# Kernel optimization log

Hardware: AMD Instinct MI355X
Metric: run time of the kernel (lower is better)

Reference implementation:

```python
import jax, jax.numpy as jnp
import numpy as np

B, N, D, H = 2, 2048, 1024, 16
HD = D // H  # 64
EPS = 1e-6


def setup_inputs() -> dict:
    key = jax.random.key(0)
    ks = jax.random.split(key, 16)
    rnd = lambda k, shp: jax.random.normal(k, shp, dtype=jnp.float32)
    w = lambda k, i, o: rnd(k, (i, o)) * 0.02  # stored as (in, out); y = x @ W
    return {
        "x": rnd(ks[0], (B, N, D)),
        "emb_B_D": rnd(ks[1], (B, D)),
        "gate": rnd(ks[2], (B, D)),
        "crossattn_emb": rnd(ks[3], (B, 128, D)),
        "rope_emb_L_1_1_D": rnd(ks[4], (N, HD)),
        "Wq1": w(ks[5], D, D), "Wq2": w(ks[6], D, D),
        "Wk1": w(ks[7], D, D), "Wk2": w(ks[8], D, D),
        "Wv": w(ks[9], D, D),
        "Wo": w(ks[10], D, D),
        "Wada1": w(ks[11], D, D),
        "Wada2": w(ks[12], D, 2 * D),
        "bada2": jnp.zeros((2 * D,), dtype=jnp.float32),
    }


def rotate_half(t):
    t1, t2 = jnp.split(t, 2, axis=-1)
    return jnp.concatenate([-t2, t1], axis=-1)


def reference(x, emb_B_D, gate, crossattn_emb, rope_emb_L_1_1_D,
              Wq1, Wq2, Wk1, Wk2, Wv, Wo, Wada1, Wada2, bada2):
    # adaLN modulation: SiLU -> Linear(no bias) -> Linear(bias)
    ada = jax.nn.silu(emb_B_D) @ Wada1 @ Wada2 + bada2          # [B, 2D]
    shift, scale = jnp.split(ada, 2, axis=1)                    # [B, D] each

    # LayerNorm (no affine) + scale/shift
    mu = jnp.mean(x, axis=-1, keepdims=True)
    var = jnp.var(x, axis=-1, keepdims=True)
    xn = (x - mu) * jax.lax.rsqrt(var + EPS)
    xn = xn * (1.0 + scale[:, None, :]) + shift[:, None, :]     # [B, N, D]

    # QKV projections (each to_q/to_k is two stacked linears, to_v one)
    q = xn @ Wq1 @ Wq2
    k = xn @ Wk1 @ Wk2
    v = xn @ Wv
    split_heads = lambda t: t.reshape(B, N, H, HD).transpose(0, 2, 1, 3)  # b h n d
    q, k, v = split_heads(q), split_heads(k), split_heads(v)

    # RoPE
    cos = jnp.cos(rope_emb_L_1_1_D)[None, None]                 # [1,1,N,HD]
    sin = jnp.sin(rope_emb_L_1_1_D)[None, None]
    q = q * cos + rotate_half(q) * sin
    k = k * cos + rotate_half(k) * sin

    # Attention
    sim = jnp.einsum("bhid,bhjd->bhij", q, k) * (HD ** -0.5)
    attn = jax.nn.softmax(sim, axis=-1)
    out = jnp.einsum("bhij,bhjd->bhid", attn, v)
    out = out.transpose(0, 2, 1, 3).reshape(B, N, D) @ Wo

    # Gated residual
    return x + gate[:, None, :] * out
```

## Files before the change

### kernel.cpp

```cpp
#include <hip/hip_runtime.h>
#include <stdint.h>
#include <math.h>

typedef unsigned short u16;
typedef __attribute__((ext_vector_type(8))) short short8;
typedef __attribute__((ext_vector_type(4))) float f32x4;
typedef __attribute__((ext_vector_type(4))) unsigned short u16x4;
typedef __attribute__((ext_vector_type(2))) unsigned int uint2v;

#define DEV static __device__ __forceinline__

DEV u16 f2bf(float f) {
    unsigned u = __builtin_bit_cast(unsigned, f);
    u = u + 0x7fffu + ((u >> 16) & 1u);
    return (u16)(u >> 16);
}
DEV float bf2f(u16 s) { return __builtin_bit_cast(float, ((unsigned)s) << 16); }
DEV unsigned pk2(float a, float b) {
    unsigned ua = __builtin_bit_cast(unsigned, a) + 0x8000u;
    unsigned ub = __builtin_bit_cast(unsigned, b) + 0x8000u;
    return (ua >> 16) | (ub & 0xffff0000u);
}
DEV float fexp2(float x) {
#if __has_builtin(__builtin_amdgcn_exp2f)
    return __builtin_amdgcn_exp2f(x);
#else
    return __expf(x * 0.69314718056f);
#endif
}

DEV void gl_lds16(const u16* g, u16* l) {
#if __has_builtin(__builtin_amdgcn_global_load_lds)
    __builtin_amdgcn_global_load_lds((const __attribute__((address_space(1))) unsigned int*)g,
                                     (__attribute__((address_space(3))) unsigned int*)l, 16, 0, 0);
#else
    *(short8*)l = *(const short8*)g;
#endif
}


__global__ __launch_bounds__(256) void k_ada1(const float* __restrict__ emb, const float* __restrict__ W,
                                              float* __restrict__ out) {
    int col = blockIdx.x * 64 + (threadIdx.x & 63);
    int b = blockIdx.y;
    int kbase = blockIdx.z * 128 + (threadIdx.x >> 6) * 32;
    float acc = 0.f;
    for (int k = kbase; k < kbase + 32; k++) {
        float e = emb[b * 1024 + k];
        float se = e / (1.f + __expf(-e));
        acc += se * W[(size_t)k * 1024 + col];
    }
    __shared__ float red[4][64];
    red[threadIdx.x >> 6][threadIdx.x & 63] = acc;
    __syncthreads();
    if (threadIdx.x < 64)
        atomicAdd(out + b * 1024 + blockIdx.x * 64 + threadIdx.x,
                  red[0][threadIdx.x] + red[1][threadIdx.x] + red[2][threadIdx.x] + red[3][threadIdx.x]);
}

__global__ __launch_bounds__(256) void k_prep(const float* s0, u16* d0, const float* s1, u16* d1,
                                              const float* s2, u16* d2, const float* s3, u16* d3,
                                              const float* s4, u16* d4, const float* s5, u16* d5,
                                              const float* __restrict__ t_ada, const float* __restrict__ Wada2,
                                              float* __restrict__ ada, const float* __restrict__ rope,
                                              float* __restrict__ cst, float* __restrict__ snt) {
    __shared__ u16 tile[64][65];
    __shared__ float red[4][64];
    if (blockIdx.z == 6) {
        int flat = blockIdx.y * 16 + blockIdx.x;
        int kq = flat >> 6;
        int rest = flat & 63;
        int b = rest >> 5, xb = rest & 31;
        int col = xb * 64 + (threadIdx.x & 63);
        int kbase = kq * 256 + (threadIdx.x >> 6) * 64;
        float acc = 0.f;
        for (int k = kbase; k < kbase + 64; k++)
            acc += t_ada[b * 1024 + k] * Wada2[(size_t)k * 2048 + col];
        red[threadIdx.x >> 6][threadIdx.x & 63] = acc;
        __syncthreads();
        if (threadIdx.x < 64)
            atomicAdd(ada + b * 2048 + xb * 64 + threadIdx.x,
                      red[0][threadIdx.x] + red[1][threadIdx.x] + red[2][threadIdx.x] + red[3][threadIdx.x]);
        return;
    }
    if (blockIdx.z == 7) {
        int flat = blockIdx.y * 16 + blockIdx.x;
        if (flat < 128) {
            int idx = flat * 1024 + threadIdx.x * 4;
            float4 rv = *(const float4*)(rope + idx);
            float4 cv, sv;
            __sincosf(rv.x, &sv.x, &cv.x);
            __sincosf(rv.y, &sv.y, &cv.y);
            __sincosf(rv.z, &sv.z, &cv.z);
            __sincosf(rv.w, &sv.w, &cv.w);
            *(float4*)(cst + idx) = cv;
            *(float4*)(snt + idx) = sv;
        }
        return;
    }
    const float* s; u16* d;
    switch (blockIdx.z) {
        case 0: s = s0; d = d0; break;
        case 1: s = s1; d = d1; break;
        case 2: s = s2; d = d2; break;
        case 3: s = s3; d = d3; break;
        case 4: s = s4; d = d4; break;
        default: s = s5; d = d5; break;
    }
    int k0 = blockIdx.x * 64, n0 = blockIdx.y * 64;
    int tx = threadIdx.x & 63, ty = threadIdx.x >> 6;
    if (blockIdx.z >= 4) {
        #pragma unroll
        for (int i = 0; i < 16; i++) {
            int kk = ty + 4 * i;
            d[(size_t)(k0 + kk) * 1024 + n0 + tx] = f2bf(s[(size_t)(k0 + kk) * 1024 + n0 + tx]);
        }
        return;
    }
    #pragma unroll
    for (int i = 0; i < 16; i++) {
        int kk = ty + 4 * i;
        tile[kk][tx] = f2bf(s[(size_t)(k0 + kk) * 1024 + n0 + tx]);
    }
    __syncthreads();
    #pragma unroll
    for (int i = 0; i < 16; i++) {
        int nn = ty + 4 * i;
        d[(size_t)(n0 + nn) * 1024 + k0 + tx] = tile[tx][nn];
    }
}

__global__ __launch_bounds__(256) void k_ln(const float* __restrict__ x, const float* __restrict__ ada,
                                            const float* __restrict__ bada2, u16* __restrict__ xn) {
    int row = blockIdx.x;
    int b = row >> 11;
    float4 v = ((const float4*)(x + (size_t)row * 1024))[threadIdx.x];
    float s = v.x + v.y + v.z + v.w;
    float ss = v.x * v.x + v.y * v.y + v.z * v.z + v.w * v.w;
    #pragma unroll
    for (int m = 1; m < 64; m <<= 1) { s += __shfl_xor(s, m, 64); ss += __shfl_xor(ss, m, 64); }
    __shared__ float red[2][4];
    int wave = threadIdx.x >> 6, lane = threadIdx.x & 63;
    if (lane == 0) { red[0][wave] = s; red[1][wave] = ss; }
    __syncthreads();
    s = red[0][0] + red[0][1] + red[0][2] + red[0][3];
    ss = red[1][0] + red[1][1] + red[1][2] + red[1][3];
    float mu = s * (1.f / 1024.f);
    float var = ss * (1.f / 1024.f) - mu * mu;
    float rs = rsqrtf(var + 1e-6f);
    int c = threadIdx.x * 4;
    const float* sh = ada + b * 2048;
    const float* sc = ada + b * 2048 + 1024;
    u16x4 r;
    r.x = f2bf((v.x - mu) * rs * (1.f + sc[c + 0] + bada2[1024 + c + 0]) + sh[c + 0] + bada2[c + 0]);
    r.y = f2bf((v.y - mu) * rs * (1.f + sc[c + 1] + bada2[1024 + c + 1]) + sh[c + 1] + bada2[c + 1]);
    r.z = f2bf((v.z - mu) * rs * (1.f + sc[c + 2] + bada2[1024 + c + 2]) + sh[c + 2] + bada2[c + 2]);
    r.w = f2bf((v.w - mu) * rs * (1.f + sc[c + 3] + bada2[1024 + c + 3]) + sh[c + 3] + bada2[c + 3]);
    *(u16x4*)(xn + (size_t)row * 1024 + c) = r;
}

template <int BM, int BN, int MODE>
DEV void gemm_core(const u16* __restrict__ A, const u16* __restrict__ Bt,
                   u16* __restrict__ Cb, float* __restrict__ Cf, u16* __restrict__ Vt,
                   const float* __restrict__ Xres, const float* __restrict__ gate,
                   const float* __restrict__ cst, const float* __restrict__ snt,
                   float scale, int Nn, int K, int m0, int n0) {
    constexpr int MI = BM / 32, NJ = BN / 32;
    constexpr int PA = BM / 64, PB = BN / 64;
    constexpr int LA = BM * 40, LB = BN * 40;
    __shared__ u16 smem[2 * (LA + LB)];
    int tid = threadIdx.x;
    int lane = tid & 63, wave = tid >> 6;
    int wm = (wave & 1) * (BM / 2), wn = (wave >> 1) * (BN / 2);
    int lr = lane & 15, quad = lane >> 4;
    f32x4 acc[MI][NJ];
    #pragma unroll
    for (int i = 0; i < MI; i++)
        #pragma unroll
        for (int j = 0; j < NJ; j++) acc[i][j] = f32x4{0.f, 0.f, 0.f, 0.f};

    int arow = tid >> 2;
    int achunk = (tid & 3) * 8;
    const u16* ap = A + (size_t)(m0 + arow) * K + achunk;
    const u16* bp = Bt + (size_t)(n0 + arow) * K + achunk;
    u16* AsL[2] = { smem, smem + LA };
    u16* BsL[2] = { smem + 2 * LA, smem + 2 * LA + LB };

    short8 ra[2][PA], rb[2][PB];
    #pragma unroll
    for (int p = 0; p < PA; p++) ra[0][p] = *(const short8*)(ap + (size_t)(64 * p) * K);
    #pragma unroll
    for (int p = 0; p < PB; p++) rb[0][p] = *(const short8*)(bp + (size_t)(64 * p) * K);
    #pragma unroll
    for (int p = 0; p < PA; p++) *(short8*)(&AsL[0][(arow + 64 * p) * 40 + achunk]) = ra[0][p];
    #pragma unroll
    for (int p = 0; p < PB; p++) *(short8*)(&BsL[0][(arow + 64 * p) * 40 + achunk]) = rb[0][p];
    #pragma unroll
    for (int p = 0; p < PA; p++) ra[1][p] = *(const short8*)(ap + 32 + (size_t)(64 * p) * K);
    #pragma unroll
    for (int p = 0; p < PB; p++) rb[1][p] = *(const short8*)(bp + 32 + (size_t)(64 * p) * K);
    __syncthreads();

    auto body = [&](int it, int cur) {
        if (it + 2 < 32) {
            int koff = (it + 2) * 32;
            #pragma unroll
            for (int p = 0; p < PA; p++) ra[cur][p] = *(const short8*)(ap + koff + (size_t)(64 * p) * K);
            #pragma unroll
            for (int p = 0; p < PB; p++) rb[cur][p] = *(const short8*)(bp + koff + (size_t)(64 * p) * K);
        }
        short8 af[MI], bfr[NJ];
        #pragma unroll
        for (int i = 0; i < MI; i++) af[i] = *(const short8*)(&AsL[cur][(wm + i * 16 + lr) * 40 + quad * 8]);
        #pragma unroll
        for (int j = 0; j < NJ; j++) bfr[j] = *(const short8*)(&BsL[cur][(wn + j * 16 + lr) * 40 + quad * 8]);
        #pragma unroll
        for (int i = 0; i < MI; i++)
            #pragma unroll
            for (int j = 0; j < NJ; j++)
                acc[i][j] = __builtin_amdgcn_mfma_f32_16x16x32_bf16(af[i], bfr[j], acc[i][j], 0, 0, 0);
        if (it + 1 < 32) {
            int nxt = cur ^ 1;
            #pragma unroll
            for (int p = 0; p < PA; p++) *(short8*)(&AsL[nxt][(arow + 64 * p) * 40 + achunk]) = ra[nxt][p];
            #pragma unroll
            for (int p = 0; p < PB; p++) *(short8*)(&BsL[nxt][(arow + 64 * p) * 40 + achunk]) = rb[nxt][p];
        }
        __syncthreads();
    };
    #pragma unroll 1
    for (int it2 = 0; it2 < 16; ++it2) {
        body(2 * it2, 0);
        body(2 * it2 + 1, 1);
    }

    if (MODE == 2) {
        if ((n0 + wn) < 2048) {
            #pragma unroll
            for (int i = 0; i < MI; i++)
                #pragma unroll
                for (int jp = 0; jp < 2; jp++)
                    #pragma unroll
                    for (int r = 0; r < 4; r++) {
                        int row = m0 + wm + i * 16 + quad * 4 + r;
                        int n = row & 2047;
                        int d1 = jp * 16 + lr;
                        float c1 = cst[n * 64 + d1],      s1 = snt[n * 64 + d1];
                        float c2 = cst[n * 64 + d1 + 32], s2 = snt[n * 64 + d1 + 32];
                        float x1 = acc[i][jp][r], x2 = acc[i][jp + 2][r];
                        Cb[(size_t)row * Nn + n0 + wn + d1]      = f2bf(x1 * c1 - x2 * s1);
                        Cb[(size_t)row * Nn + n0 + wn + d1 + 32] = f2bf(x2 * c2 + x1 * s2);
                    }
        } else {
            #pragma unroll
            for (int i = 0; i < MI; i++)
                #pragma unroll
                for (int j = 0; j < NJ; j++) {
                    u16x4 w;
                    w.x = f2bf(acc[i][j][0]); w.y = f2bf(acc[i][j][1]);
                    w.z = f2bf(acc[i][j][2]); w.w = f2bf(acc[i][j][3]);
                    *(u16x4*)(&smem[(wn + j * 16 + lr) * 132 + wm + i * 16 + quad * 4]) = w;
                }
            __syncthreads();
            int d = tid >> 1, half = tid & 1;
            int gcol = n0 - 2048 + d;
            int hv = gcol >> 6, dl = gcol & 63;
            int bb = m0 >> 11;
            int nloc = (m0 & 2047) + half * 64;
            u16* dst = Vt + ((size_t)((bb * 16 + hv) * 64 + dl)) * 2048 + nloc;
            #pragma unroll
            for (int c = 0; c < 8; c++)
                *(short8*)(dst + c * 8) = *(const short8*)(&smem[d * 132 + half * 64 + c * 8]);
        }
        return;
    }
    #pragma unroll
    for (int i = 0; i < MI; i++)
        #pragma unroll
        for (int j = 0; j < NJ; j++)
            #pragma unroll
            for (int r = 0; r < 4; r++) {
                int row = m0 + wm + i * 16 + quad * 4 + r;
                int col = n0 + wn + j * 16 + lr;
                float v = acc[i][j][r];
                if (MODE == 1) {
                    int b = row >> 11;
                    Cf[(size_t)row * Nn + col] = Xres[(size_t)row * Nn + col] + gate[b * 1024 + col] * v;
                } else {
                    Cb[(size_t)row * Nn + col] = f2bf(v * scale);
                }
            }
}

template <int BM, int BN, int MODE, int WPE>
__global__ __launch_bounds__(256, WPE) void gemm_bt(const u16* __restrict__ A, const u16* __restrict__ Bt,
                                                    u16* __restrict__ Cb, float* __restrict__ Cf,
                                                    u16* __restrict__ Vt,
                                                    const float* __restrict__ Xres, const float* __restrict__ gate,
                                                    const float* __restrict__ cst, const float* __restrict__ snt,
                                                    int Nn, int K) {
    gemm_core<BM, BN, MODE>(A, Bt, Cb, Cf, Vt, Xres, gate, cst, snt, 1.f, Nn, K,
                            blockIdx.y * BM, blockIdx.x * BN);
}

__global__ __launch_bounds__(256, 4) void gemm_fold(const u16* A0, const u16* B0, u16* C0,
                                                    const u16* A1, const u16* B1, u16* C1) {
    const u16* A = blockIdx.z ? A1 : A0;
    const u16* Bt = blockIdx.z ? B1 : B0;
    u16* C = blockIdx.z ? C1 : C0;
    float scale = blockIdx.z ? 1.0f : 0.18033688f;
    gemm_core<128, 64, 0>(A, Bt, C, nullptr, nullptr, nullptr, nullptr, nullptr, nullptr, scale,
                          1024, 1024, blockIdx.y * 128, blockIdx.x * 64);
}

__global__ __launch_bounds__(512) void k_attn(const u16* __restrict__ qkv, const u16* __restrict__ vt,
                                              u16* __restrict__ aob) {
    __shared__ u16 pool[128 * 72];
    __shared__ u16 Ks[2][64][64];
    __shared__ u16 Vs[2][64][64];
    int q0 = blockIdx.x * 128;
    int bh = blockIdx.y; int b = bh >> 4, h = bh & 15;
    int tid = threadIdx.x;
    int lane = tid & 63, wave = tid >> 6;
    int lr = lane & 15, quad = lane >> 4;
    int srow = tid >> 3, scol = (tid & 7) * 8;
    int sg = (((tid & 7) ^ (srow & 7))) * 8;
    int cc[2] = { ((quad ^ (lr & 7))) * 8, (((4 + quad) ^ (lr & 7))) * 8 };
    int qrow = wave * 16 + lr;

    const u16* kp = qkv + ((size_t)(b * 2048 + srow)) * 2048 + 1024 + h * 64 + sg;
    const u16* vp = vt + ((size_t)(bh * 64 + srow)) * 2048 + sg;

    #pragma unroll
    for (int p = 0; p < 2; p++)
        gl_lds16(qkv + ((size_t)(b * 2048 + q0 + srow + 64 * p)) * 2048 + h * 64 + sg,
                 pool + (srow + 64 * p) * 64 + scol);

    short8 krA, vrA, krB, vrB;
    krA = *(const short8*)(kp);
    vrA = *(const short8*)(vp);
    __syncthreads();
    short8 qf[2];
    #pragma unroll
    for (int ks = 0; ks < 2; ks++)
        qf[ks] = *(const short8*)(pool + qrow * 64 + cc[ks]);
    *(short8*)(&Ks[0][srow][scol]) = krA;
    *(short8*)(&Vs[0][srow][scol]) = vrA;
    krB = *(const short8*)(kp + (size_t)64 * 2048);
    vrB = *(const short8*)(vp + 64);
    __syncthreads();

    float l_part = 0.f;
    f32x4 oacc[4];
    #pragma unroll
    for (int dt = 0; dt < 4; dt++) oacc[dt] = f32x4{0.f, 0.f, 0.f, 0.f};

    auto body = [&](int it, int cur, short8& krF, short8& vrF, short8& krH, short8& vrH) {
        if (it < 30) {
            krF = *(const short8*)(kp + (size_t)(it + 2) * 64 * 2048);
            vrF = *(const short8*)(vp + (it + 2) * 64);
        }
        f32x4 st[4];
        #pragma unroll
        for (int ct = 0; ct < 4; ct++) st[ct] = f32x4{0.f, 0.f, 0.f, 0.f};
        #pragma unroll
        for (int ks = 0; ks < 2; ks++) {
            short8 kf[4];
            #pragma unroll
            for (int ct = 0; ct < 4; ct++)
                kf[ct] = *(const short8*)(&Ks[cur][ct * 16 + lr][cc[ks]]);
            __builtin_amdgcn_s_setprio(1);
            #pragma unroll
            for (int ct = 0; ct < 4; ct++)
                st[ct] = __builtin_amdgcn_mfma_f32_16x16x32_bf16(kf[ct], qf[ks], st[ct], 0, 0, 0);
            __builtin_amdgcn_s_setprio(0);
        }
        #pragma unroll
        for (int ct = 0; ct < 4; ct++) {
            float p0 = fexp2(st[ct][0]);
            float p1 = fexp2(st[ct][1]);
            float p2 = fexp2(st[ct][2]);
            float p3 = fexp2(st[ct][3]);
            l_part += (p0 + p1) + (p2 + p3);
            uint2v w; w.x = pk2(p0, p1); w.y = pk2(p2, p3);
            *(uint2v*)(pool + qrow * 72 + ct * 16 + quad * 4) = w;
        }
        #pragma unroll
        for (int ks = 0; ks < 2; ks++) {
            short8 pf, vf[4];
            pf = *(const short8*)(pool + qrow * 72 + ks * 32 + quad * 8);
            #pragma unroll
            for (int dt = 0; dt < 4; dt++)
                vf[dt] = *(const short8*)(&Vs[cur][dt * 16 + lr][cc[ks]]);
            __builtin_amdgcn_s_setprio(1);
            #pragma unroll
            for (int dt = 0; dt < 4; dt++)
                oacc[dt] = __builtin_amdgcn_mfma_f32_16x16x32_bf16(pf, vf[dt], oacc[dt], 0, 0, 0);
            __builtin_amdgcn_s_setprio(0);
        }
        if (it < 31) {
            int nxt = cur ^ 1;
            *(short8*)(&Ks[nxt][srow][scol]) = krH;
            *(short8*)(&Vs[nxt][srow][scol]) = vrH;
        }
        __syncthreads();
    };

    #pragma unroll 1
    for (int it2 = 0; it2 < 16; ++it2) {
        body(2 * it2,     0, krA, vrA, krB, vrB);
        body(2 * it2 + 1, 1, krB, vrB, krA, vrA);
    }

    float l = l_part;
    l += __shfl_xor(l, 16, 64);
    l += __shfl_xor(l, 32, 64);
    float linv[4];
    #pragma unroll
    for (int r = 0; r < 4; r++)
        linv[r] = 1.f / __shfl(l, quad * 4 + r, 64);
    #pragma unroll
    for (int dt = 0; dt < 4; dt++)
        #pragma unroll
        for (int r = 0; r < 4; r++) {
            int row = q0 + wave * 16 + quad * 4 + r;
            aob[((size_t)(b * 2048 + row)) * 1024 + h * 64 + dt * 16 + lr] =
                f2bf(oacc[dt][r] * linv[r]);
        }
}

extern "C" void kernel_launch(void* const* d_in, const int* in_sizes, int n_in,
                              void* d_out, int out_size, void* d_ws, size_t ws_size,
                              hipStream_t stream) {
    const float* x     = (const float*)d_in[0];
    const float* emb   = (const float*)d_in[1];
    const float* gate  = (const float*)d_in[2];
    const float* rope  = (const float*)d_in[4];
    const float* Wq1   = (const float*)d_in[5];
    const float* Wq2   = (const float*)d_in[6];
    const float* Wk1   = (const float*)d_in[7];
    const float* Wk2   = (const float*)d_in[8];
    const float* Wv    = (const float*)d_in[9];
    const float* Wo    = (const float*)d_in[10];
    const float* Wada1 = (const float*)d_in[11];
    const float* Wada2 = (const float*)d_in[12];
    const float* bada2 = (const float*)d_in[13];
    float* out = (float*)d_out;

    char* ws = (char*)d_ws;
    size_t off = 0;
    auto alloc = [&](size_t bytes) { void* p = ws + off; off += (bytes + 255) & ~(size_t)255; return p; };
    float* t_ada = (float*)alloc(2048 * 4);
    float* ada   = (float*)alloc(4096 * 4);
    float* cst   = (float*)alloc((size_t)131072 * 4);
    float* snt   = (float*)alloc((size_t)131072 * 4);
    u16* xn    = (u16*)alloc((size_t)4096 * 1024 * 2);
    u16* Wq1b  = (u16*)alloc((size_t)1024 * 1024 * 2);
    u16* Wk1b  = (u16*)alloc((size_t)1024 * 1024 * 2);
    u16* Wq2t  = (u16*)alloc((size_t)1024 * 1024 * 2);
    u16* Wk2t  = (u16*)alloc((size_t)1024 * 1024 * 2);
    u16* Wot   = (u16*)alloc((size_t)1024 * 1024 * 2);
    u16* WqkvT = (u16*)alloc((size_t)3072 * 1024 * 2);
    u16* qkvb  = (u16*)alloc((size_t)4096 * 2048 * 2);
    u16* vtb   = (u16*)alloc((size_t)4096 * 1024 * 2);
    u16* aob   = (u16*)alloc((size_t)4096 * 1024 * 2);
    (void)ws_size; (void)in_sizes; (void)n_in; (void)out_size;

    hipMemsetAsync(t_ada, 0, 2048 * 4, stream);
    hipMemsetAsync(ada, 0, 4096 * 4, stream);

    k_ada1<<<dim3(16, 2, 8), 256, 0, stream>>>(emb, Wada1, t_ada);

    k_prep<<<dim3(16, 16, 8), 256, 0, stream>>>(Wq2, Wq2t, Wk2, Wk2t,
                                                Wv, WqkvT + (size_t)2048 * 1024, Wo, Wot,
                                                Wq1, Wq1b, Wk1, Wk1b,
                                                t_ada, Wada2, ada, rope, cst, snt);

    k_ln<<<4096, 256, 0, stream>>>(x, ada, bada2, xn);

    gemm_fold<<<dim3(16, 8, 2), 256, 0, stream>>>(Wq2t, Wq1b, WqkvT,
                                                  Wk2t, Wk1b, WqkvT + (size_t)1024 * 1024);

    gemm_bt<128, 128, 2, 3><<<dim3(24, 32), 256, 0, stream>>>(xn, WqkvT, qkvb, nullptr, vtb,
                                                              nullptr, nullptr, cst, snt, 2048, 1024);

    k_attn<<<dim3(16, 32), 512, 0, stream>>>(qkvb, vtb, aob);

    gemm_bt<128, 64, 1, 4><<<dim3(16, 32), 256, 0, stream>>>(aob, Wot, nullptr, out, nullptr, x, gate,
                                                             nullptr, nullptr, 1024, 1024);
}
```

Measured before the change: 263.1 us.

## Software-pipeline attention loop: overlap previous tile's PV with current QK

```diff
diff --git a/kernel.cpp b/kernel.cpp
--- a/kernel.cpp
+++ b/kernel.cpp
@@ -316,8 +316,8 @@
 __global__ __launch_bounds__(512) void k_attn(const u16* __restrict__ qkv, const u16* __restrict__ vt,
                                               u16* __restrict__ aob) {
     __shared__ u16 pool[128 * 72];
-    __shared__ u16 Ks[2][64][64];
-    __shared__ u16 Vs[2][64][64];
+    __shared__ u16 Ks[3][64][64];
+    __shared__ u16 Vs[3][64][64];
     int q0 = blockIdx.x * 128;
     int bh = blockIdx.y; int b = bh >> 4, h = bh & 15;
     int tid = threadIdx.x;
@@ -355,26 +355,42 @@
     #pragma unroll
     for (int dt = 0; dt < 4; dt++) oacc[dt] = f32x4{0.f, 0.f, 0.f, 0.f};
 
-    auto body = [&](int it, int cur, short8& krF, short8& vrF, short8& krH, short8& vrH) {
-        if (it < 30) {
-            krF = *(const short8*)(kp + (size_t)(it + 2) * 64 * 2048);
-            vrF = *(const short8*)(vp + (it + 2) * 64);
-        }
+    auto pv_step = [&](int vbuf) {
+        #pragma unroll
+        for (int ks = 0; ks < 2; ks++) {
+            short8 pf = *(const short8*)(pool + qrow * 72 + ks * 32 + quad * 8);
+            short8 vf[4];
+            #pragma unroll
+            for (int dt = 0; dt < 4; dt++)
+                vf[dt] = *(const short8*)(&Vs[vbuf][dt * 16 + lr][cc[ks]]);
+            #pragma unroll
+            for (int dt = 0; dt < 4; dt++)
+                oacc[dt] = __builtin_amdgcn_mfma_f32_16x16x32_bf16(pf, vf[dt], oacc[dt], 0, 0, 0);
+        }
+    };
+
+    auto body = [&](int t, short8& krF, short8& vrF, short8& krH, short8& vrH) {
+        if (t < 30) {
+            krF = *(const short8*)(kp + (size_t)(t + 2) * 64 * 2048);
+            vrF = *(const short8*)(vp + (t + 2) * 64);
+        }
+        int cur3 = t % 3, nxt3 = (t + 1) % 3, prv3 = (t + 2) % 3;
         f32x4 st[4];
         #pragma unroll
         for (int ct = 0; ct < 4; ct++) st[ct] = f32x4{0.f, 0.f, 0.f, 0.f};
+        __builtin_amdgcn_s_setprio(1);
         #pragma unroll
         for (int ks = 0; ks < 2; ks++) {
             short8 kf[4];
             #pragma unroll
             for (int ct = 0; ct < 4; ct++)
-                kf[ct] = *(const short8*)(&Ks[cur][ct * 16 + lr][cc[ks]]);
-            __builtin_amdgcn_s_setprio(1);
+                kf[ct] = *(const short8*)(&Ks[cur3][ct * 16 + lr][cc[ks]]);
             #pragma unroll
             for (int ct = 0; ct < 4; ct++)
                 st[ct] = __builtin_amdgcn_mfma_f32_16x16x32_bf16(kf[ct], qf[ks], st[ct], 0, 0, 0);
-            __builtin_amdgcn_s_setprio(0);
-        }
+        }
+        if (t > 0) pv_step(prv3);
+        __builtin_amdgcn_s_setprio(0);
         #pragma unroll
         for (int ct = 0; ct < 4; ct++) {
             float p0 = fexp2(st[ct][0]);
@@ -385,32 +401,19 @@
             uint2v w; w.x = pk2(p0, p1); w.y = pk2(p2, p3);
             *(uint2v*)(pool + qrow * 72 + ct * 16 + quad * 4) = w;
         }
-        #pragma unroll
-        for (int ks = 0; ks < 2; ks++) {
-            short8 pf, vf[4];
-            pf = *(const short8*)(pool + qrow * 72 + ks * 32 + quad * 8);
-            #pragma unroll
-            for (int dt = 0; dt < 4; dt++)
-                vf[dt] = *(const short8*)(&Vs[cur][dt * 16 + lr][cc[ks]]);
-            __builtin_amdgcn_s_setprio(1);
-            #pragma unroll
-            for (int dt = 0; dt < 4; dt++)
-                oacc[dt] = __builtin_amdgcn_mfma_f32_16x16x32_bf16(pf, vf[dt], oacc[dt], 0, 0, 0);
-            __builtin_amdgcn_s_setprio(0);
-        }
-        if (it < 31) {
-            int nxt = cur ^ 1;
-            *(short8*)(&Ks[nxt][srow][scol]) = krH;
-            *(short8*)(&Vs[nxt][srow][scol]) = vrH;
+        if (t < 31) {
+            *(short8*)(&Ks[nxt3][srow][scol]) = krH;
+            *(short8*)(&Vs[nxt3][srow][scol]) = vrH;
         }
         __syncthreads();
     };
 
     #pragma unroll 1
     for (int it2 = 0; it2 < 16; ++it2) {
-        body(2 * it2,     0, krA, vrA, krB, vrB);
-        body(2 * it2 + 1, 1, krB, vrB, krA, vrA);
-    }
+        body(2 * it2,     krA, vrA, krB, vrB);
+        body(2 * it2 + 1, krB, vrB, krA, vrA);
+    }
+    pv_step(1);
 
     float l = l_part;
     l += __shfl_xor(l, 16, 64);
```

Measured after the change: 264.7 us. About the same (+0.6%).

## Stage GEMM tiles via direct global-to-LDS loads and use hardware bf16 pack

Applied to the files above, without the earlier changes.

```diff
diff --git a/kernel.cpp b/kernel.cpp
--- a/kernel.cpp
+++ b/kernel.cpp
@@ -16,17 +16,17 @@
     return (u16)(u >> 16);
 }
 DEV float bf2f(u16 s) { return __builtin_bit_cast(float, ((unsigned)s) << 16); }
-DEV unsigned pk2(float a, float b) {
-    unsigned ua = __builtin_bit_cast(unsigned, a) + 0x8000u;
-    unsigned ub = __builtin_bit_cast(unsigned, b) + 0x8000u;
-    return (ua >> 16) | (ub & 0xffff0000u);
-}
 DEV float fexp2(float x) {
 #if __has_builtin(__builtin_amdgcn_exp2f)
     return __builtin_amdgcn_exp2f(x);
 #else
     return __expf(x * 0.69314718056f);
 #endif
+}
+DEV unsigned cvtpk(float a, float b) {
+    unsigned w;
+    asm("v_cvt_pk_bf16_f32 %0, %1, %2" : "=v"(w) : "v"(a), "v"(b));
+    return w;
 }
 
 DEV void gl_lds16(const u16* g, u16* l) {
@@ -167,8 +167,10 @@
                    float scale, int Nn, int K, int m0, int n0) {
     constexpr int MI = BM / 32, NJ = BN / 32;
     constexpr int PA = BM / 64, PB = BN / 64;
-    constexpr int LA = BM * 40, LB = BN * 40;
-    __shared__ u16 smem[2 * (LA + LB)];
+    constexpr int LA = BM * 32, LB = BN * 32;
+    constexpr int SST = 2 * (LA + LB);
+    constexpr int SM = (MODE == 2 && BM * 132 > SST) ? BM * 132 : SST;
+    __shared__ u16 smem[SM];
     int tid = threadIdx.x;
     int lane = tid & 63, wave = tid >> 6;
     int wm = (wave & 1) * (BM / 2), wn = (wave >> 1) * (BN / 2);
@@ -183,55 +185,38 @@
     int achunk = (tid & 3) * 8;
     const u16* ap = A + (size_t)(m0 + arow) * K + achunk;
     const u16* bp = Bt + (size_t)(n0 + arow) * K + achunk;
-    u16* AsL[2] = { smem, smem + LA };
-    u16* BsL[2] = { smem + 2 * LA, smem + 2 * LA + LB };
-
-    short8 ra[2][PA], rb[2][PB];
-    #pragma unroll
-    for (int p = 0; p < PA; p++) ra[0][p] = *(const short8*)(ap + (size_t)(64 * p) * K);
-    #pragma unroll
-    for (int p = 0; p < PB; p++) rb[0][p] = *(const short8*)(bp + (size_t)(64 * p) * K);
-    #pragma unroll
-    for (int p = 0; p < PA; p++) *(short8*)(&AsL[0][(arow + 64 * p) * 40 + achunk]) = ra[0][p];
-    #pragma unroll
-    for (int p = 0; p < PB; p++) *(short8*)(&BsL[0][(arow + 64 * p) * 40 + achunk]) = rb[0][p];
-    #pragma unroll
-    for (int p = 0; p < PA; p++) ra[1][p] = *(const short8*)(ap + 32 + (size_t)(64 * p) * K);
-    #pragma unroll
-    for (int p = 0; p < PB; p++) rb[1][p] = *(const short8*)(bp + 32 + (size_t)(64 * p) * K);
-    __syncthreads();
-
-    auto body = [&](int it, int cur) {
-        if (it + 2 < 32) {
-            int koff = (it + 2) * 32;
-            #pragma unroll
-            for (int p = 0; p < PA; p++) ra[cur][p] = *(const short8*)(ap + koff + (size_t)(64 * p) * K);
-            #pragma unroll
-            for (int p = 0; p < PB; p++) rb[cur][p] = *(const short8*)(bp + koff + (size_t)(64 * p) * K);
-        }
+
+    auto stage = [&](int it, int d) {
+        int koff = it * 32;
+        int ab = d * LA, bb = 2 * LA + d * LB;
+        #pragma unroll
+        for (int p = 0; p < PA; p++)
+            gl_lds16(ap + koff + (size_t)(64 * p) * K, smem + ab + (arow + 64 * p) * 32 + achunk);
+        #pragma unroll
+        for (int p = 0; p < PB; p++)
+            gl_lds16(bp + koff + (size_t)(64 * p) * K, smem + bb + (arow + 64 * p) * 32 + achunk);
+    };
+
+    stage(0, 0);
+    __syncthreads();
+    #pragma unroll 1
+    for (int it = 0; it < 32; ++it) {
+        int cur = it & 1;
+        if (it + 1 < 32) stage(it + 1, cur ^ 1);
+        int ab = cur * LA, bb = 2 * LA + cur * LB;
         short8 af[MI], bfr[NJ];
         #pragma unroll
-        for (int i = 0; i < MI; i++) af[i] = *(const short8*)(&AsL[cur][(wm + i * 16 + lr) * 40 + quad * 8]);
-        #pragma unroll
-        for (int j = 0; j < NJ; j++) bfr[j] = *(const short8*)(&BsL[cur][(wn + j * 16 + lr) * 40 + quad * 8]);
+        for (int i = 0; i < MI; i++)
+            af[i] = *(const short8*)(smem + ab + (wm + i * 16 + lr) * 32 + quad * 8);
+        #pragma unroll
+        for (int j = 0; j < NJ; j++)
+            bfr[j] = *(const short8*)(smem + bb + (wn + j * 16 + lr) * 32 + quad * 8);
         #pragma unroll
         for (int i = 0; i < MI; i++)
             #pragma unroll
             for (int j = 0; j < NJ; j++)
                 acc[i][j] = __builtin_amdgcn_mfma_f32_16x16x32_bf16(af[i], bfr[j], acc[i][j], 0, 0, 0);
-        if (it + 1 < 32) {
-            int nxt = cur ^ 1;
-            #pragma unroll
-            for (int p = 0; p < PA; p++) *(short8*)(&AsL[nxt][(arow + 64 * p) * 40 + achunk]) = ra[nxt][p];
-            #pragma unroll
-            for (int p = 0; p < PB; p++) *(short8*)(&BsL[nxt][(arow + 64 * p) * 40 + achunk]) = rb[nxt][p];
-        }
         __syncthreads();
-    };
-    #pragma unroll 1
-    for (int it2 = 0; it2 < 16; ++it2) {
-        body(2 * it2, 0);
-        body(2 * it2 + 1, 1);
     }
 
     if (MODE == 2) {
@@ -265,9 +250,9 @@
             int d = tid >> 1, half = tid & 1;
             int gcol = n0 - 2048 + d;
             int hv = gcol >> 6, dl = gcol & 63;
-            int bb = m0 >> 11;
+            int bb2 = m0 >> 11;
             int nloc = (m0 & 2047) + half * 64;
-            u16* dst = Vt + ((size_t)((bb * 16 + hv) * 64 + dl)) * 2048 + nloc;
+            u16* dst = Vt + ((size_t)((bb2 * 16 + hv) * 64 + dl)) * 2048 + nloc;
             #pragma unroll
             for (int c = 0; c < 8; c++)
                 *(short8*)(dst + c * 8) = *(const short8*)(&smem[d * 132 + half * 64 + c * 8]);
@@ -382,7 +367,7 @@
             float p2 = fexp2(st[ct][2]);
             float p3 = fexp2(st[ct][3]);
             l_part += (p0 + p1) + (p2 + p3);
-            uint2v w; w.x = pk2(p0, p1); w.y = pk2(p2, p3);
+            uint2v w; w.x = cvtpk(p0, p1); w.y = cvtpk(p2, p3);
             *(uint2v*)(pool + qrow * 72 + ct * 16 + quad * 4) = w;
         }
         #pragma unroll
@@ -481,7 +466,7 @@
     gemm_fold<<<dim3(16, 8, 2), 256, 0, stream>>>(Wq2t, Wq1b, WqkvT,
                                                   Wk2t, Wk1b, WqkvT + (size_t)1024 * 1024);
 
-    gemm_bt<128, 128, 2, 3><<<dim3(24, 32), 256, 0, stream>>>(xn, WqkvT, qkvb, nullptr, vtb,
+    gemm_bt<128, 128, 2, 4><<<dim3(24, 32), 256, 0, stream>>>(xn, WqkvT, qkvb, nullptr, vtb,
                                                               nullptr, nullptr, cst, snt, 2048, 1024);
 
     k_attn<<<dim3(16, 32), 512, 0, stream>>>(qkvb, vtb, aob);
```

Measured after the change: 257.3 us. 2.2% less time.
